# Kernel optimization log

Hardware: AMD Instinct MI355X
Metric: run time of the kernel (lower is better)

The kernel has to match this reference:

```python
import jax, jax.numpy as jnp
import numpy as np

DIM = 1024
HEADS = 16

def setup_inputs() -> dict:
    key = jax.random.key(0)
    k1, k2 = jax.random.split(key)
    x = jax.random.normal(k1, (4, 2048, DIM), dtype=jnp.float32)
    # torch nn.Linear(dim, 3*dim, bias=False): weight shape [3*dim, dim], y = x @ W.T
    W_qkv = jax.random.normal(k2, (3 * DIM, DIM), dtype=jnp.float32) * (DIM ** -0.5)
    return {"x": x, "W_qkv": W_qkv}

def reference(x, W_qkv):
    B, N, D = x.shape
    H = HEADS
    hd = D // H
    scale = hd ** -0.5
    qkv = jnp.einsum('bnd,ed->bne', x, W_qkv)            # [B,N,3D]
    qkv = qkv.reshape(B, N, 3, H, hd).transpose(2, 0, 3, 1, 4)  # [3,B,H,N,hd]
    q, k, v = qkv[0], qkv[1], qkv[2]
    attn = jnp.einsum('bhnd,bhmd->bhnm', q, k) * scale   # [B,H,N,N]
    attn = jax.nn.softmax(attn, axis=-1)                 # dropout is identity at eval
    out = jnp.einsum('bhnm,bhmd->bhnd', attn, v)         # [B,H,N,hd]
    return out.transpose(0, 2, 1, 3).reshape(B, N, D)
```

## Files before the change

kernel.cpp:

```cpp
#include <hip/hip_runtime.h>

typedef unsigned short ushort_t;
typedef short bf16x8 __attribute__((ext_vector_type(8)));
typedef float f32x4 __attribute__((ext_vector_type(4)));
typedef float f32x16 __attribute__((ext_vector_type(16)));

__device__ __forceinline__ unsigned f2bf(float f) {
  union { float f; unsigned u; } v; v.f = f;
  return (v.u + 0x7FFFu + ((v.u >> 16) & 1u)) >> 16;
}

__device__ __forceinline__ void gll16(const void* g, const void* l) {
  __builtin_amdgcn_global_load_lds(
      (const __attribute__((address_space(1))) void*)g,
      (__attribute__((address_space(3))) void*)l, 16, 0, 0);
}

__global__ __launch_bounds__(256) void cvt_bf16(const float* __restrict__ src,
                                                ushort_t* __restrict__ dst, int n4) {
  int i = blockIdx.x * 256 + threadIdx.x;
  if (i >= n4) return;
  float4 v = ((const float4*)src)[i];
  uint2 o;
  o.x = f2bf(v.x) | (f2bf(v.y) << 16);
  o.y = f2bf(v.z) | (f2bf(v.w) << 16);
  ((uint2*)dst)[i] = o;
}

__global__ __launch_bounds__(256) void gemm_qkv(const ushort_t* __restrict__ A,
                                                const ushort_t* __restrict__ Bw,
                                                ushort_t* __restrict__ C) {
  __shared__ ushort_t As[128 * 64];
  __shared__ ushort_t Bs[128 * 64];
  const int tid = threadIdx.x;
  const int w = tid >> 6, ln = tid & 63;
  const int g = ln >> 4, lr = ln & 15;
  const int bx = blockIdx.x;
  const int nt = bx % 24, mt = bx / 24;
  const int m0 = mt * 128, n0 = nt * 128;
  const int wr = w >> 1, wc = w & 1;
  const float cscale = (nt < 8) ? 0.18033688f : 1.0f;

  f32x4 acc[4][4] = {};

  for (int kt = 0; kt < 16; ++kt) {
#pragma unroll
    for (int q = 0; q < 4; ++q) {
      int chunk = w * 256 + q * 64 + ln;
      int r = chunk >> 3, c = chunk & 7;
      int cs = c ^ (r & 7);
      gll16(A + (size_t)(m0 + r) * 1024 + kt * 64 + cs * 8, As + chunk * 8);
      gll16(Bw + (size_t)(n0 + r) * 1024 + kt * 64 + cs * 8, Bs + chunk * 8);
    }
    __syncthreads();
#pragma unroll
    for (int ks = 0; ks < 2; ++ks) {
      bf16x8 af[4], bfr[4];
#pragma unroll
      for (int mi = 0; mi < 4; ++mi) {
        int row = wr * 64 + mi * 16 + lr;
        af[mi] = *(const bf16x8*)((const char*)As + row * 128 +
                                  ((g * 16 + ks * 64) ^ ((row & 7) << 4)));
      }
#pragma unroll
      for (int ni = 0; ni < 4; ++ni) {
        int row = wc * 64 + ni * 16 + lr;
        bfr[ni] = *(const bf16x8*)((const char*)Bs + row * 128 +
                                   ((g * 16 + ks * 64) ^ ((row & 7) << 4)));
      }
#pragma unroll
      for (int mi = 0; mi < 4; ++mi)
#pragma unroll
        for (int ni = 0; ni < 4; ++ni)
          acc[mi][ni] = __builtin_amdgcn_mfma_f32_16x16x32_bf16(af[mi], bfr[ni],
                                                                acc[mi][ni], 0, 0, 0);
    }
    __syncthreads();
  }

#pragma unroll
  for (int mi = 0; mi < 4; ++mi)
#pragma unroll
    for (int ni = 0; ni < 4; ++ni)
#pragma unroll
      for (int r = 0; r < 4; ++r) {
        int row = m0 + wr * 64 + mi * 16 + g * 4 + r;
        int col = n0 + wc * 64 + ni * 16 + lr;
        C[(size_t)row * 3072 + col] = (ushort_t)f2bf(acc[mi][ni][r] * cscale);
      }
}

__global__ __launch_bounds__(256) void vtrans(const ushort_t* __restrict__ qkv,
                                              ushort_t* __restrict__ VT) {
  __shared__ ushort_t tl[64][72];
  int blk = blockIdx.x;
  int bh = blk >> 5, nb = blk & 31;
  int b = bh >> 4, h = bh & 15;
  int t = threadIdx.x;
  int r = t >> 2, c = t & 3;
  const ushort_t* src = qkv + (size_t)(b * 2048 + nb * 64 + r) * 3072 + 2048 + h * 64 + c * 16;
  uint2 v0 = *(const uint2*)(src);
  uint2 v1 = *(const uint2*)(src + 4);
  uint2 v2 = *(const uint2*)(src + 8);
  uint2 v3 = *(const uint2*)(src + 12);
  *(uint2*)&tl[r][c * 16] = v0;
  *(uint2*)&tl[r][c * 16 + 4] = v1;
  *(uint2*)&tl[r][c * 16 + 8] = v2;
  *(uint2*)&tl[r][c * 16 + 12] = v3;
  __syncthreads();
  int d = t >> 2, dc = t & 3;
  unsigned pk[8];
#pragma unroll
  for (int j = 0; j < 8; ++j) {
    unsigned lo = tl[dc * 16 + 2 * j][d];
    unsigned hi = tl[dc * 16 + 2 * j + 1][d];
    pk[j] = lo | (hi << 16);
  }
  ushort_t* dst = VT + (size_t)(bh * 64 + d) * 2048 + nb * 64 + dc * 16;
  uint4 o0; o0.x = pk[0]; o0.y = pk[1]; o0.z = pk[4]; o0.w = pk[5];
  uint4 o1; o1.x = pk[2]; o1.y = pk[3]; o1.z = pk[6]; o1.w = pk[7];
  *(uint4*)dst = o0;
  *(uint4*)(dst + 8) = o1;
}

__global__ __launch_bounds__(256, 4) void attn2(const ushort_t* __restrict__ qkv,
                                                const ushort_t* __restrict__ VT,
                                                float* __restrict__ out) {
  __shared__ ushort_t Ks[3][32 * 64];
  __shared__ ushort_t Vs[3][32 * 64];
  const int blk = blockIdx.x;
  const int bh = blk & 63, qt = blk >> 6;
  const int b = bh >> 4, hh = bh & 15;
  const int tid = threadIdx.x;
  const int w = tid >> 6, l = tid & 63;
  const int q = l & 31, h = l >> 5;
  const int q0 = qt * 128 + w * 32;

  const ushort_t* qrow = qkv + (size_t)(b * 2048 + q0 + q) * 3072 + hh * 64 + 8 * h;
  bf16x8 qf[4];
#pragma unroll
  for (int m = 0; m < 4; ++m) qf[m] = *(const bf16x8*)(qrow + 16 * m);

  union { ushort_t s[8]; bf16x8 v; } vones;
#pragma unroll
  for (int i = 0; i < 8; ++i) vones.s[i] = 0x3F80;

  const int rS = tid >> 3, cS = tid & 7;
  const int cL = cS ^ (rS & 7);
  const ushort_t* srcK =
      qkv + (size_t)(b * 2048 + rS) * 3072 + 1024 + hh * 64 + cL * 8;
  const ushort_t* srcV =
      VT + (size_t)(bh * 64 + rS + 32 * (cL >> 2)) * 2048 + (cL & 3) * 8;

  f32x16 oacc0, oacc1, lacc;
#pragma unroll
  for (int i = 0; i < 16; ++i) { oacc0[i] = 0.f; oacc1[i] = 0.f; lacc[i] = 0.f; }

  gll16(srcK, &Ks[0][tid * 8]);
  gll16(srcV, &Vs[0][tid * 8]);
  gll16(srcK + (size_t)32 * 3072, &Ks[1][tid * 8]);
  gll16(srcV + 32, &Vs[1][tid * 8]);
  asm volatile("s_waitcnt vmcnt(2)" ::: "memory");
  __builtin_amdgcn_s_barrier();

  int cur = 0;
  for (int t = 0; t < 64; ++t) {
    int tn = t + 2; if (tn > 63) tn = 63;
    int bufn = cur + 2; if (bufn >= 3) bufn -= 3;
    gll16(srcK + (size_t)tn * 32 * 3072, &Ks[bufn][tid * 8]);
    gll16(srcV + tn * 32, &Vs[bufn][tid * 8]);

    const ushort_t* KsB = Ks[cur];
    const ushort_t* VsB = Vs[cur];

    f32x16 S;
#pragma unroll
    for (int i = 0; i < 16; ++i) S[i] = 0.f;
    __builtin_amdgcn_s_setprio(1);
#pragma unroll
    for (int m = 0; m < 4; ++m) {
      bf16x8 kf = *(const bf16x8*)(KsB + q * 64 + (((2 * m + h) ^ (q & 7)) * 8));
      S = __builtin_amdgcn_mfma_f32_32x32x16_bf16(kf, qf[m], S, 0, 0, 0);
    }
    __builtin_amdgcn_s_setprio(0);

    float p[16];
#pragma unroll
    for (int i = 0; i < 16; ++i) p[i] = __builtin_amdgcn_exp2f(S[i]);

    union { unsigned u[4]; bf16x8 v; } pf0, pf1;
#pragma unroll
    for (int i = 0; i < 4; ++i)
      asm("v_cvt_pk_bf16_f32 %0, %1, %2"
          : "=v"(pf0.u[i]) : "v"(p[2 * i]), "v"(p[2 * i + 1]));
#pragma unroll
    for (int i = 0; i < 4; ++i)
      asm("v_cvt_pk_bf16_f32 %0, %1, %2"
          : "=v"(pf1.u[i]) : "v"(p[8 + 2 * i]), "v"(p[8 + 2 * i + 1]));

    bf16x8 vf0 = *(const bf16x8*)(VsB + q * 64 + (((0 + h) ^ (q & 7)) * 8));
    bf16x8 vf1 = *(const bf16x8*)(VsB + q * 64 + (((2 + h) ^ (q & 7)) * 8));
    bf16x8 vf2 = *(const bf16x8*)(VsB + q * 64 + (((4 + h) ^ (q & 7)) * 8));
    bf16x8 vf3 = *(const bf16x8*)(VsB + q * 64 + (((6 + h) ^ (q & 7)) * 8));

    __builtin_amdgcn_s_setprio(1);
    oacc0 = __builtin_amdgcn_mfma_f32_32x32x16_bf16(vf0, pf0.v, oacc0, 0, 0, 0);
    oacc0 = __builtin_amdgcn_mfma_f32_32x32x16_bf16(vf1, pf1.v, oacc0, 0, 0, 0);
    oacc1 = __builtin_amdgcn_mfma_f32_32x32x16_bf16(vf2, pf0.v, oacc1, 0, 0, 0);
    oacc1 = __builtin_amdgcn_mfma_f32_32x32x16_bf16(vf3, pf1.v, oacc1, 0, 0, 0);
    lacc  = __builtin_amdgcn_mfma_f32_32x32x16_bf16(vones.v, pf0.v, lacc, 0, 0, 0);
    lacc  = __builtin_amdgcn_mfma_f32_32x32x16_bf16(vones.v, pf1.v, lacc, 0, 0, 0);
    __builtin_amdgcn_s_setprio(0);

    asm volatile("s_waitcnt vmcnt(2)" ::: "memory");
    __builtin_amdgcn_s_barrier();
    cur += 1; if (cur == 3) cur = 0;
  }

  float inv = 1.0f / lacc[0];
  float* orow = out + (size_t)(b * 2048 + q0 + q) * 1024 + hh * 64 + 4 * h;
#pragma unroll
  for (int rq = 0; rq < 4; ++rq) {
    float4 o0, o1;
    o0.x = oacc0[rq * 4 + 0] * inv; o0.y = oacc0[rq * 4 + 1] * inv;
    o0.z = oacc0[rq * 4 + 2] * inv; o0.w = oacc0[rq * 4 + 3] * inv;
    o1.x = oacc1[rq * 4 + 0] * inv; o1.y = oacc1[rq * 4 + 1] * inv;
    o1.z = oacc1[rq * 4 + 2] * inv; o1.w = oacc1[rq * 4 + 3] * inv;
    *(float4*)(orow + 8 * rq) = o0;
    *(float4*)(orow + 32 + 8 * rq) = o1;
  }
}

extern "C" void kernel_launch(void* const* d_in, const int* in_sizes, int n_in,
                              void* d_out, int out_size, void* d_ws, size_t ws_size,
                              hipStream_t stream) {
  const float* x = (const float*)d_in[0];
  const float* Wq = (const float*)d_in[1];
  float* out = (float*)d_out;
  char* ws = (char*)d_ws;

  ushort_t* xb = (ushort_t*)ws;
  ushort_t* wb = (ushort_t*)(ws + 16777216);
  ushort_t* qkv = (ushort_t*)(ws + 23068672);
  ushort_t* VT = xb;

  cvt_bf16<<<8192, 256, 0, stream>>>(x, xb, 8192 * 1024 / 4);
  cvt_bf16<<<3072, 256, 0, stream>>>(Wq, wb, 3072 * 1024 / 4);
  gemm_qkv<<<64 * 24, 256, 0, stream>>>(xb, wb, qkv);
  vtrans<<<64 * 32, 256, 0, stream>>>(qkv, VT);
  attn2<<<64 * 16, 256, 0, stream>>>(qkv, VT, out);
}
```

Before: 176.4 us.

## Process 64-key tiles per barrier and compute softmax row sums with VALU adds

Each pipeline stage now loads and processes two 32-key sub-tiles, which halves the number of barriers and waitcnt points across the K/V loop and doubles the LDS buffer size per stage. The row-sum of exponentials is computed with float adds plus a cross-half shuffle instead of two extra MFMAs against a ones vector. This cuts matrix-core work by a third and reduces synchronisation, at the cost of more LDS per block (which may affect occupancy) and extra VALU and shuffle work.

```diff
diff --git a/kernel.cpp b/kernel.cpp
--- a/kernel.cpp
+++ b/kernel.cpp
@@ -123,11 +123,50 @@
   *(uint4*)(dst + 8) = o1;
 }
 
+#define SUBTILE(KSB, VSB, LSOUT)                                              \
+  {                                                                           \
+    const ushort_t* KB = (KSB);                                               \
+    const ushort_t* VB = (VSB);                                               \
+    f32x16 S;                                                                 \
+    _Pragma("unroll") for (int i = 0; i < 16; ++i) S[i] = 0.f;                \
+    __builtin_amdgcn_s_setprio(1);                                            \
+    _Pragma("unroll") for (int m = 0; m < 4; ++m) {                           \
+      bf16x8 kf = *(const bf16x8*)(KB + q * 64 + (((2 * m + h) ^ qsw) * 8));  \
+      S = __builtin_amdgcn_mfma_f32_32x32x16_bf16(kf, qf[m], S, 0, 0, 0);     \
+    }                                                                         \
+    __builtin_amdgcn_s_setprio(0);                                            \
+    float p[16];                                                              \
+    _Pragma("unroll") for (int i = 0; i < 16; ++i)                            \
+      p[i] = __builtin_amdgcn_exp2f(S[i]);                                    \
+    float s0 = (p[0] + p[1]) + (p[2] + p[3]);                                 \
+    float s1 = (p[4] + p[5]) + (p[6] + p[7]);                                 \
+    float s2 = (p[8] + p[9]) + (p[10] + p[11]);                               \
+    float s3 = (p[12] + p[13]) + (p[14] + p[15]);                             \
+    LSOUT = (s0 + s1) + (s2 + s3);                                            \
+    union { unsigned u[4]; bf16x8 v; } pf0, pf1;                              \
+    _Pragma("unroll") for (int i = 0; i < 4; ++i)                             \
+      asm("v_cvt_pk_bf16_f32 %0, %1, %2"                                      \
+          : "=v"(pf0.u[i]) : "v"(p[2 * i]), "v"(p[2 * i + 1]));               \
+    _Pragma("unroll") for (int i = 0; i < 4; ++i)                             \
+      asm("v_cvt_pk_bf16_f32 %0, %1, %2"                                      \
+          : "=v"(pf1.u[i]) : "v"(p[8 + 2 * i]), "v"(p[8 + 2 * i + 1]));       \
+    bf16x8 vf0 = *(const bf16x8*)(VB + q * 64 + (((0 + h) ^ qsw) * 8));       \
+    bf16x8 vf1 = *(const bf16x8*)(VB + q * 64 + (((2 + h) ^ qsw) * 8));       \
+    bf16x8 vf2 = *(const bf16x8*)(VB + q * 64 + (((4 + h) ^ qsw) * 8));       \
+    bf16x8 vf3 = *(const bf16x8*)(VB + q * 64 + (((6 + h) ^ qsw) * 8));       \
+    __builtin_amdgcn_s_setprio(1);                                            \
+    oacc0 = __builtin_amdgcn_mfma_f32_32x32x16_bf16(vf0, pf0.v, oacc0, 0, 0, 0); \
+    oacc0 = __builtin_amdgcn_mfma_f32_32x32x16_bf16(vf1, pf1.v, oacc0, 0, 0, 0); \
+    oacc1 = __builtin_amdgcn_mfma_f32_32x32x16_bf16(vf2, pf0.v, oacc1, 0, 0, 0); \
+    oacc1 = __builtin_amdgcn_mfma_f32_32x32x16_bf16(vf3, pf1.v, oacc1, 0, 0, 0); \
+    __builtin_amdgcn_s_setprio(0);                                            \
+  }
+
 __global__ __launch_bounds__(256, 4) void attn2(const ushort_t* __restrict__ qkv,
                                                 const ushort_t* __restrict__ VT,
                                                 float* __restrict__ out) {
-  __shared__ ushort_t Ks[3][32 * 64];
-  __shared__ ushort_t Vs[3][32 * 64];
+  __shared__ ushort_t Ks[3][4096];
+  __shared__ ushort_t Vs[3][4096];
   const int blk = blockIdx.x;
   const int bh = blk & 63, qt = blk >> 6;
   const int b = bh >> 4, hh = bh & 15;
@@ -135,15 +174,12 @@
   const int w = tid >> 6, l = tid & 63;
   const int q = l & 31, h = l >> 5;
   const int q0 = qt * 128 + w * 32;
+  const int qsw = q & 7;
 
   const ushort_t* qrow = qkv + (size_t)(b * 2048 + q0 + q) * 3072 + hh * 64 + 8 * h;
   bf16x8 qf[4];
 #pragma unroll
   for (int m = 0; m < 4; ++m) qf[m] = *(const bf16x8*)(qrow + 16 * m);
-
-  union { ushort_t s[8]; bf16x8 v; } vones;
-#pragma unroll
-  for (int i = 0; i < 8; ++i) vones.s[i] = 0x3F80;
 
   const int rS = tid >> 3, cS = tid & 7;
   const int cL = cS ^ (rS & 7);
@@ -152,72 +188,44 @@
   const ushort_t* srcV =
       VT + (size_t)(bh * 64 + rS + 32 * (cL >> 2)) * 2048 + (cL & 3) * 8;
 
-  f32x16 oacc0, oacc1, lacc;
-#pragma unroll
-  for (int i = 0; i < 16; ++i) { oacc0[i] = 0.f; oacc1[i] = 0.f; lacc[i] = 0.f; }
-
-  gll16(srcK, &Ks[0][tid * 8]);
-  gll16(srcV, &Vs[0][tid * 8]);
-  gll16(srcK + (size_t)32 * 3072, &Ks[1][tid * 8]);
-  gll16(srcV + 32, &Vs[1][tid * 8]);
-  asm volatile("s_waitcnt vmcnt(2)" ::: "memory");
+  f32x16 oacc0, oacc1;
+#pragma unroll
+  for (int i = 0; i < 16; ++i) { oacc0[i] = 0.f; oacc1[i] = 0.f; }
+  float l_run = 0.f;
+
+  gll16(srcK, Ks[0] + tid * 8);
+  gll16(srcK + (size_t)32 * 3072, Ks[0] + 2048 + tid * 8);
+  gll16(srcV, Vs[0] + tid * 8);
+  gll16(srcV + 32, Vs[0] + 2048 + tid * 8);
+  gll16(srcK + (size_t)64 * 3072, Ks[1] + tid * 8);
+  gll16(srcK + (size_t)96 * 3072, Ks[1] + 2048 + tid * 8);
+  gll16(srcV + 64, Vs[1] + tid * 8);
+  gll16(srcV + 96, Vs[1] + 2048 + tid * 8);
+  asm volatile("s_waitcnt vmcnt(4)" ::: "memory");
   __builtin_amdgcn_s_barrier();
 
   int cur = 0;
-  for (int t = 0; t < 64; ++t) {
-    int tn = t + 2; if (tn > 63) tn = 63;
+  for (int tt = 0; tt < 32; ++tt) {
+    int tn = tt + 2; if (tn > 31) tn = 31;
     int bufn = cur + 2; if (bufn >= 3) bufn -= 3;
-    gll16(srcK + (size_t)tn * 32 * 3072, &Ks[bufn][tid * 8]);
-    gll16(srcV + tn * 32, &Vs[bufn][tid * 8]);
-
-    const ushort_t* KsB = Ks[cur];
-    const ushort_t* VsB = Vs[cur];
-
-    f32x16 S;
-#pragma unroll
-    for (int i = 0; i < 16; ++i) S[i] = 0.f;
-    __builtin_amdgcn_s_setprio(1);
-#pragma unroll
-    for (int m = 0; m < 4; ++m) {
-      bf16x8 kf = *(const bf16x8*)(KsB + q * 64 + (((2 * m + h) ^ (q & 7)) * 8));
-      S = __builtin_amdgcn_mfma_f32_32x32x16_bf16(kf, qf[m], S, 0, 0, 0);
-    }
-    __builtin_amdgcn_s_setprio(0);
-
-    float p[16];
-#pragma unroll
-    for (int i = 0; i < 16; ++i) p[i] = __builtin_amdgcn_exp2f(S[i]);
-
-    union { unsigned u[4]; bf16x8 v; } pf0, pf1;
-#pragma unroll
-    for (int i = 0; i < 4; ++i)
-      asm("v_cvt_pk_bf16_f32 %0, %1, %2"
-          : "=v"(pf0.u[i]) : "v"(p[2 * i]), "v"(p[2 * i + 1]));
-#pragma unroll
-    for (int i = 0; i < 4; ++i)
-      asm("v_cvt_pk_bf16_f32 %0, %1, %2"
-          : "=v"(pf1.u[i]) : "v"(p[8 + 2 * i]), "v"(p[8 + 2 * i + 1]));
-
-    bf16x8 vf0 = *(const bf16x8*)(VsB + q * 64 + (((0 + h) ^ (q & 7)) * 8));
-    bf16x8 vf1 = *(const bf16x8*)(VsB + q * 64 + (((2 + h) ^ (q & 7)) * 8));
-    bf16x8 vf2 = *(const bf16x8*)(VsB + q * 64 + (((4 + h) ^ (q & 7)) * 8));
-    bf16x8 vf3 = *(const bf16x8*)(VsB + q * 64 + (((6 + h) ^ (q & 7)) * 8));
-
-    __builtin_amdgcn_s_setprio(1);
-    oacc0 = __builtin_amdgcn_mfma_f32_32x32x16_bf16(vf0, pf0.v, oacc0, 0, 0, 0);
-    oacc0 = __builtin_amdgcn_mfma_f32_32x32x16_bf16(vf1, pf1.v, oacc0, 0, 0, 0);
-    oacc1 = __builtin_amdgcn_mfma_f32_32x32x16_bf16(vf2, pf0.v, oacc1, 0, 0, 0);
-    oacc1 = __builtin_amdgcn_mfma_f32_32x32x16_bf16(vf3, pf1.v, oacc1, 0, 0, 0);
-    lacc  = __builtin_amdgcn_mfma_f32_32x32x16_bf16(vones.v, pf0.v, lacc, 0, 0, 0);
-    lacc  = __builtin_amdgcn_mfma_f32_32x32x16_bf16(vones.v, pf1.v, lacc, 0, 0, 0);
-    __builtin_amdgcn_s_setprio(0);
-
-    asm volatile("s_waitcnt vmcnt(2)" ::: "memory");
+    gll16(srcK + (size_t)(2 * tn) * 32 * 3072, Ks[bufn] + tid * 8);
+    gll16(srcK + (size_t)(2 * tn + 1) * 32 * 3072, Ks[bufn] + 2048 + tid * 8);
+    gll16(srcV + (2 * tn) * 32, Vs[bufn] + tid * 8);
+    gll16(srcV + (2 * tn + 1) * 32, Vs[bufn] + 2048 + tid * 8);
+
+    float ls0, ls1;
+    SUBTILE(Ks[cur], Vs[cur], ls0);
+    SUBTILE(Ks[cur] + 2048, Vs[cur] + 2048, ls1);
+    float ls = ls0 + ls1;
+    ls += __shfl_xor(ls, 32, 64);
+    l_run += ls;
+
+    asm volatile("s_waitcnt vmcnt(4)" ::: "memory");
     __builtin_amdgcn_s_barrier();
     cur += 1; if (cur == 3) cur = 0;
   }
 
-  float inv = 1.0f / lacc[0];
+  float inv = 1.0f / l_run;
   float* orow = out + (size_t)(b * 2048 + q0 + q) * 1024 + hh * 64 + 4 * h;
 #pragma unroll
   for (int rq = 0; rq < 4; ++rq) {
```

After: 184.5 us. 4.6% more time.

## Double attention block size and replace ones-MFMA row sum with VALU reduction

Applied to the files above, without the earlier changes.

The attention kernel now runs 512-thread blocks covering 256 query rows, so each K/V tile staged in shared memory serves twice as many queries. Half the threads load K and half load V, one load each per step. The softmax denominator is now a per-lane VALU sum plus a cross-half shuffle instead of two extra MFMAs against a ones vector. This cuts MFMA work and global-to-LDS traffic per query, but halves the grid to 512 blocks and removes the occupancy hint from the launch bounds.

```diff
diff --git a/kernel.cpp b/kernel.cpp
--- a/kernel.cpp
+++ b/kernel.cpp
@@ -123,52 +123,50 @@
   *(uint4*)(dst + 8) = o1;
 }
 
-__global__ __launch_bounds__(256, 4) void attn2(const ushort_t* __restrict__ qkv,
-                                                const ushort_t* __restrict__ VT,
-                                                float* __restrict__ out) {
-  __shared__ ushort_t Ks[3][32 * 64];
-  __shared__ ushort_t Vs[3][32 * 64];
+__global__ __launch_bounds__(512) void attn2(const ushort_t* __restrict__ qkv,
+                                             const ushort_t* __restrict__ VT,
+                                             float* __restrict__ out) {
+  __shared__ ushort_t Ks[3][2048];
+  __shared__ ushort_t Vs[3][2048];
   const int blk = blockIdx.x;
   const int bh = blk & 63, qt = blk >> 6;
   const int b = bh >> 4, hh = bh & 15;
   const int tid = threadIdx.x;
   const int w = tid >> 6, l = tid & 63;
   const int q = l & 31, h = l >> 5;
-  const int q0 = qt * 128 + w * 32;
+  const int q0 = qt * 256 + w * 32;
+  const int qsw = q & 7;
 
   const ushort_t* qrow = qkv + (size_t)(b * 2048 + q0 + q) * 3072 + hh * 64 + 8 * h;
   bf16x8 qf[4];
 #pragma unroll
   for (int m = 0; m < 4; ++m) qf[m] = *(const bf16x8*)(qrow + 16 * m);
 
-  union { ushort_t s[8]; bf16x8 v; } vones;
-#pragma unroll
-  for (int i = 0; i < 8; ++i) vones.s[i] = 0x3F80;
-
-  const int rS = tid >> 3, cS = tid & 7;
+  const int st = tid & 255;
+  const int rS = st >> 3, cS = st & 7;
   const int cL = cS ^ (rS & 7);
-  const ushort_t* srcK =
-      qkv + (size_t)(b * 2048 + rS) * 3072 + 1024 + hh * 64 + cL * 8;
-  const ushort_t* srcV =
-      VT + (size_t)(bh * 64 + rS + 32 * (cL >> 2)) * 2048 + (cL & 3) * 8;
-
-  f32x16 oacc0, oacc1, lacc;
-#pragma unroll
-  for (int i = 0; i < 16; ++i) { oacc0[i] = 0.f; oacc1[i] = 0.f; lacc[i] = 0.f; }
-
-  gll16(srcK, &Ks[0][tid * 8]);
-  gll16(srcV, &Vs[0][tid * 8]);
-  gll16(srcK + (size_t)32 * 3072, &Ks[1][tid * 8]);
-  gll16(srcV + 32, &Vs[1][tid * 8]);
-  asm volatile("s_waitcnt vmcnt(2)" ::: "memory");
+  const bool isK = tid < 256;
+  const ushort_t* gsrc =
+      isK ? qkv + (size_t)(b * 2048 + rS) * 3072 + 1024 + hh * 64 + cL * 8
+          : VT + (size_t)(bh * 64 + rS + 32 * (cL >> 2)) * 2048 + (cL & 3) * 8;
+  const size_t gstep = isK ? (size_t)32 * 3072 : (size_t)32;
+  ushort_t* lbase = isK ? &Ks[0][0] : &Vs[0][0];
+
+  f32x16 oacc0, oacc1;
+#pragma unroll
+  for (int i = 0; i < 16; ++i) { oacc0[i] = 0.f; oacc1[i] = 0.f; }
+  float l_run = 0.f;
+
+  gll16(gsrc, lbase + st * 8);
+  gll16(gsrc + gstep, lbase + 2048 + st * 8);
+  asm volatile("s_waitcnt vmcnt(1)" ::: "memory");
   __builtin_amdgcn_s_barrier();
 
   int cur = 0;
   for (int t = 0; t < 64; ++t) {
     int tn = t + 2; if (tn > 63) tn = 63;
     int bufn = cur + 2; if (bufn >= 3) bufn -= 3;
-    gll16(srcK + (size_t)tn * 32 * 3072, &Ks[bufn][tid * 8]);
-    gll16(srcV + tn * 32, &Vs[bufn][tid * 8]);
+    gll16(gsrc + (size_t)tn * gstep, lbase + bufn * 2048 + st * 8);
 
     const ushort_t* KsB = Ks[cur];
     const ushort_t* VsB = Vs[cur];
@@ -179,7 +177,7 @@
     __builtin_amdgcn_s_setprio(1);
 #pragma unroll
     for (int m = 0; m < 4; ++m) {
-      bf16x8 kf = *(const bf16x8*)(KsB + q * 64 + (((2 * m + h) ^ (q & 7)) * 8));
+      bf16x8 kf = *(const bf16x8*)(KsB + q * 64 + (((2 * m + h) ^ qsw) * 8));
       S = __builtin_amdgcn_mfma_f32_32x32x16_bf16(kf, qf[m], S, 0, 0, 0);
     }
     __builtin_amdgcn_s_setprio(0);
@@ -187,6 +185,13 @@
     float p[16];
 #pragma unroll
     for (int i = 0; i < 16; ++i) p[i] = __builtin_amdgcn_exp2f(S[i]);
+    float s0 = (p[0] + p[1]) + (p[2] + p[3]);
+    float s1 = (p[4] + p[5]) + (p[6] + p[7]);
+    float s2 = (p[8] + p[9]) + (p[10] + p[11]);
+    float s3 = (p[12] + p[13]) + (p[14] + p[15]);
+    float ls = (s0 + s1) + (s2 + s3);
+    ls += __shfl_xor(ls, 32, 64);
+    l_run += ls;
 
     union { unsigned u[4]; bf16x8 v; } pf0, pf1;
 #pragma unroll
@@ -198,26 +203,24 @@
       asm("v_cvt_pk_bf16_f32 %0, %1, %2"
           : "=v"(pf1.u[i]) : "v"(p[8 + 2 * i]), "v"(p[8 + 2 * i + 1]));
 
-    bf16x8 vf0 = *(const bf16x8*)(VsB + q * 64 + (((0 + h) ^ (q & 7)) * 8));
-    bf16x8 vf1 = *(const bf16x8*)(VsB + q * 64 + (((2 + h) ^ (q & 7)) * 8));
-    bf16x8 vf2 = *(const bf16x8*)(VsB + q * 64 + (((4 + h) ^ (q & 7)) * 8));
-    bf16x8 vf3 = *(const bf16x8*)(VsB + q * 64 + (((6 + h) ^ (q & 7)) * 8));
+    bf16x8 vf0 = *(const bf16x8*)(VsB + q * 64 + (((0 + h) ^ qsw) * 8));
+    bf16x8 vf1 = *(const bf16x8*)(VsB + q * 64 + (((2 + h) ^ qsw) * 8));
+    bf16x8 vf2 = *(const bf16x8*)(VsB + q * 64 + (((4 + h) ^ qsw) * 8));
+    bf16x8 vf3 = *(const bf16x8*)(VsB + q * 64 + (((6 + h) ^ qsw) * 8));
 
     __builtin_amdgcn_s_setprio(1);
     oacc0 = __builtin_amdgcn_mfma_f32_32x32x16_bf16(vf0, pf0.v, oacc0, 0, 0, 0);
     oacc0 = __builtin_amdgcn_mfma_f32_32x32x16_bf16(vf1, pf1.v, oacc0, 0, 0, 0);
     oacc1 = __builtin_amdgcn_mfma_f32_32x32x16_bf16(vf2, pf0.v, oacc1, 0, 0, 0);
     oacc1 = __builtin_amdgcn_mfma_f32_32x32x16_bf16(vf3, pf1.v, oacc1, 0, 0, 0);
-    lacc  = __builtin_amdgcn_mfma_f32_32x32x16_bf16(vones.v, pf0.v, lacc, 0, 0, 0);
-    lacc  = __builtin_amdgcn_mfma_f32_32x32x16_bf16(vones.v, pf1.v, lacc, 0, 0, 0);
     __builtin_amdgcn_s_setprio(0);
 
-    asm volatile("s_waitcnt vmcnt(2)" ::: "memory");
+    asm volatile("s_waitcnt vmcnt(1)" ::: "memory");
     __builtin_amdgcn_s_barrier();
     cur += 1; if (cur == 3) cur = 0;
   }
 
-  float inv = 1.0f / lacc[0];
+  float inv = 1.0f / l_run;
   float* orow = out + (size_t)(b * 2048 + q0 + q) * 1024 + hh * 64 + 4 * h;
 #pragma unroll
   for (int rq = 0; rq < 4; ++rq) {
@@ -248,5 +251,5 @@
   cvt_bf16<<<3072, 256, 0, stream>>>(Wq, wb, 3072 * 1024 / 4);
   gemm_qkv<<<64 * 24, 256, 0, stream>>>(xb, wb, qkv);
   vtrans<<<64 * 32, 256, 0, stream>>>(qkv, VT);
-  attn2<<<64 * 16, 256, 0, stream>>>(qkv, VT, out);
-}
+  attn2<<<64 * 8, 512, 0, stream>>>(qkv, VT, out);
+}
```

Result: faster. 170.4 us (-3.4%).
